# Performance work log

Hardware: AMD Instinct MI355X
Metric: run time of the kernel (lower is better)

Reference implementation:

```python
import jax, jax.numpy as jnp
from jax import lax
import numpy as np

IN_F, H1, OUT_F, P = 128, 64, 64, 0.25
B, T = 64, 2048


def setup_inputs() -> dict:
    key = jax.random.key(0)
    ks = jax.random.split(key, 12)
    def w(k, shape, fan_in):
        return jax.random.normal(k, shape, dtype=jnp.float32) / np.sqrt(fan_in).astype(np.float32)
    x = jax.random.normal(ks[0], (B, T, IN_F), dtype=jnp.float32)
    # PyTorch LSTM param layout: W_ih [4H, in], W_hh [4H, H], gate order i,f,g,o
    W_ih1 = w(ks[1], (4 * H1, IN_F), IN_F)
    W_hh1 = w(ks[2], (4 * H1, H1), H1)
    b_ih1 = jnp.zeros((4 * H1,), jnp.float32)
    b_hh1 = jnp.zeros((4 * H1,), jnp.float32)
    W_ih2 = w(ks[3], (4 * OUT_F, H1), H1)
    W_hh2 = w(ks[4], (4 * OUT_F, OUT_F), OUT_F)
    b_ih2 = jnp.zeros((4 * OUT_F,), jnp.float32)
    b_hh2 = jnp.zeros((4 * OUT_F,), jnp.float32)
    # Variational (locked) dropout masks: one per sequence, shared across timesteps,
    # inverted-dropout pre-scaled by 1/(1-p).
    keep = 1.0 - P
    mask1 = (jax.random.bernoulli(ks[5], keep, (B, H1)).astype(jnp.float32) / keep)
    mask2 = (jax.random.bernoulli(ks[6], keep, (B, OUT_F)).astype(jnp.float32) / keep)
    return {"x": x, "W_ih1": W_ih1, "W_hh1": W_hh1, "b_ih1": b_ih1, "b_hh1": b_hh1,
            "W_ih2": W_ih2, "W_hh2": W_hh2, "b_ih2": b_ih2, "b_hh2": b_hh2,
            "mask1": mask1, "mask2": mask2}


def _lstm(x, W_ih, W_hh, b_ih, b_hh):
    # x: [B,T,I]; returns all hidden states [B,T,H]
    Bd = x.shape[0]
    H = W_hh.shape[1]
    # Precompute input contribution for all timesteps (one big GEMM).
    xg = jnp.einsum('bti,gi->btg', x, W_ih) + b_ih + b_hh  # [B,T,4H]
    W_hh_T = W_hh.T  # [H,4H]
    def step(carry, xg_t):
        h, c = carry
        g = xg_t + h @ W_hh_T
        i, f, gg, o = jnp.split(g, 4, axis=-1)
        c = jax.nn.sigmoid(f) * c + jax.nn.sigmoid(i) * jnp.tanh(gg)
        h = jax.nn.sigmoid(o) * jnp.tanh(c)
        return (h, c), h
    h0 = jnp.zeros((Bd, H), x.dtype)
    c0 = jnp.zeros((Bd, H), x.dtype)
    _, hs = lax.scan(step, (h0, c0), jnp.swapaxes(xg, 0, 1))
    return jnp.swapaxes(hs, 0, 1)


def reference(x, W_ih1, W_hh1, b_ih1, b_hh1, W_ih2, W_hh2, b_ih2, b_hh2, mask1, mask2):
    out = _lstm(x, W_ih1, W_hh1, b_ih1, b_hh1) * mask1[:, None, :]
    out = _lstm(out, W_ih2, W_hh2, b_ih2, b_hh2) * mask2[:, None, :]
    return jax.nn.relu(out)
```

## Files before the change

kernel.cpp:

```cpp
#include <hip/hip_runtime.h>
#include <hip/hip_bf16.h>

#define BB 64
#define TT 2048
#define INF 128
#define HH 64
#define GG 256

__device__ __forceinline__ float sigm(float x) { return 1.0f / (1.0f + __expf(-x)); }
__device__ __forceinline__ float tanh_f(float x) {
  float e = __expf(2.0f * x);
  return 1.0f - 2.0f / (e + 1.0f);
}
__device__ __forceinline__ float bcast(float v, int l) {
  return __uint_as_float(__builtin_amdgcn_readlane(__float_as_uint(v), l));
}


#define WL1(I)                                                                  \
  { float4 a = p[lane * 16 + (I)];                                              \
    wi[4*(I)] = a.x; wi[4*(I)+1] = a.y; wi[4*(I)+2] = a.z; wi[4*(I)+3] = a.w;   \
    float4 c = p[(64 + lane) * 16 + (I)];                                       \
    wf[4*(I)] = c.x; wf[4*(I)+1] = c.y; wf[4*(I)+2] = c.z; wf[4*(I)+3] = c.w;   \
    float4 d = p[(128 + lane) * 16 + (I)];                                      \
    wg[4*(I)] = d.x; wg[4*(I)+1] = d.y; wg[4*(I)+2] = d.z; wg[4*(I)+3] = d.w;   \
    float4 e = p[(192 + lane) * 16 + (I)];                                      \
    wo[4*(I)] = e.x; wo[4*(I)+1] = e.y; wo[4*(I)+2] = e.z; wo[4*(I)+3] = e.w; }
#define WL4(I) WL1(I) WL1((I)+1) WL1((I)+2) WL1((I)+3)
#define WLOAD WL4(0) WL4(4) WL4(8) WL4(12)

#define D1(K)                                              \
  { float hk = bcast(hv, (K));                             \
    ai = fmaf(hk, wi[(K)], ai); af = fmaf(hk, wf[(K)], af);\
    ag = fmaf(hk, wg[(K)], ag); ao = fmaf(hk, wo[(K)], ao); }
#define D8(K) D1(K) D1((K)+1) D1((K)+2) D1((K)+3) D1((K)+4) D1((K)+5) D1((K)+6) D1((K)+7)
#define DOT64 D8(0) D8(8) D8(16) D8(24) D8(32) D8(40) D8(48) D8(56)

#define YW1(I) { float4 a_ = Wp[t * 32 + (I)];                                   \
    wr[4*(I)] = a_.x; wr[4*(I)+1] = a_.y; wr[4*(I)+2] = a_.z; wr[4*(I)+3] = a_.w; }
#define YW4(I) YW1(I) YW1((I)+1) YW1((I)+2) YW1((I)+3)
#define YWLOAD YW4(0) YW4(4) YW4(8) YW4(12) YW4(16) YW4(20) YW4(24) YW4(28)

#define YD1(L)                                                   \
  { float xa = bcast(curx, (L)); float xb = bcast(cury, (L));    \
    ae = fmaf(xa, wr[2*(L)], ae); ao = fmaf(xb, wr[2*(L)+1], ao); }
#define YD8(L) YD1(L) YD1((L)+1) YD1((L)+2) YD1((L)+3) YD1((L)+4) YD1((L)+5) YD1((L)+6) YD1((L)+7)
#define YDOT64 YD8(0) YD8(8) YD8(16) YD8(24) YD8(32) YD8(40) YD8(48) YD8(56)

__global__ __launch_bounds__(256, 1) void xgemm(const float* __restrict__ X,
                                                const float* __restrict__ W,
                                                const float* __restrict__ bi,
                                                const float* __restrict__ bh,
                                                float* __restrict__ XG) {
  const int t = threadIdx.x;
  const int lane = t & 63;
  const long m0 = (long)blockIdx.x * 256;

  float wr[INF];
  const float4* Wp = (const float4*)W;
  YWLOAD
  const float bias = bi[t] + bh[t];

  const float2* Xp = (const float2*)X;
  float2 cur = Xp[(size_t)m0 * 64 + lane];
  float2 nx1 = Xp[(size_t)(m0 + 1) * 64 + lane];

  for (int mi = 0; mi < 256; ++mi) {
    const long m = m0 + mi;
    float2 nx2 = make_float2(0.f, 0.f);
    if (mi + 2 < 256) nx2 = Xp[(size_t)(m + 2) * 64 + lane];

    const float curx = cur.x, cury = cur.y;
    float ae = bias, ao = 0.f;
    YDOT64
    XG[(size_t)m * GG + t] = ae + ao;
    cur = nx1; nx1 = nx2;
  }
}

__global__ __attribute__((amdgpu_flat_work_group_size(256, 256),
                          amdgpu_waves_per_eu(1, 1)))
void lstm2(const float* __restrict__ XG,
           const float* __restrict__ Whh1,
           const float* __restrict__ Wih2,
           const float* __restrict__ Whh2,
           const float* __restrict__ bi2,
           const float* __restrict__ bh2,
           const float* __restrict__ m1g,
           const float* __restrict__ m2g,
           float* __restrict__ out) {
  const int b = blockIdx.x;
  const int wid = threadIdx.x >> 6;
  const int lane = threadIdx.x & 63;

  __shared__ int f_h1, f_xe, f_xo, f_2;
  __shared__ __align__(16) float x2buf[8][HH];
  __shared__ __align__(16) float a2xbuf[8][GG];

  if (threadIdx.x == 0) { f_h1 = 0; f_xe = 0; f_xo = 0; f_2 = 0; }
  __syncthreads();

#define WAITC(seen, flag, tgt)                                  \
  do {                                                          \
    if ((seen) < (tgt)) {                                       \
      while (((seen) = *(volatile int*)&(flag)) < (tgt)) {}     \
    }                                                           \
    asm volatile("" ::: "memory");                              \
  } while (0)
#define PUBLISH(flag, val)                                      \
  do {                                                          \
    asm volatile("s_waitcnt lgkmcnt(0)" ::: "memory");          \
    if (lane == 0) *(volatile int*)&(flag) = (val);             \
  } while (0)

  if (wid == 0) {
    float wi[HH], wf[HH], wg[HH], wo[HH];
    const float4* p = (const float4*)Whh1;
    WLOAD
    const float m1 = m1g[b * HH + lane];
    const float* xgp = XG + (size_t)b * TT * GG;

    float cur0 = xgp[lane], cur1 = xgp[64 + lane], cur2 = xgp[128 + lane], cur3 = xgp[192 + lane];
    float n10 = xgp[GG + lane], n11 = xgp[GG + 64 + lane], n12 = xgp[GG + 128 + lane], n13 = xgp[GG + 192 + lane];

    float h1 = 0.f, c1 = 0.f;
    int sxe = 0, sxo = 0;
    for (int s = 0; s < TT; ++s) {
      float n20 = 0.f, n21 = 0.f, n22 = 0.f, n23 = 0.f;
      if (s + 2 < TT) {
        const float* q = xgp + (size_t)(s + 2) * GG;
        n20 = q[lane]; n21 = q[64 + lane]; n22 = q[128 + lane]; n23 = q[192 + lane];
      }

      const float hv = h1;
      float ai = cur0, af = cur1, ag = cur2, ao = cur3;
      DOT64
      c1 = sigm(af) * c1 + sigm(ai) * tanh_f(ag);
      h1 = sigm(ao) * tanh_f(c1);

      if (s & 1) { WAITC(sxo, f_xo, s - 7); }
      else       { WAITC(sxe, f_xe, s - 7); }
      x2buf[s & 7][lane] = h1 * m1;
      PUBLISH(f_h1, s + 1);

      cur0 = n10; cur1 = n11; cur2 = n12; cur3 = n13;
      n10 = n20; n11 = n21; n12 = n22; n13 = n23;
    }
  } else if (wid == 3) {
    float wi[HH], wf[HH], wg[HH], wo[HH];
    const float4* p = (const float4*)Whh2;
    WLOAD
    const float m2v = m2g[b * HH + lane];
    float* ob = out + (size_t)b * TT * HH;

    float h2 = 0.f, c2 = 0.f;
    int sxe = 0, sxo = 0;
    for (int s = 0; s < TT; ++s) {
      if (s & 1) { WAITC(sxo, f_xo, s + 1); }
      else       { WAITC(sxe, f_xe, s + 1); }
      const float pi = a2xbuf[s & 7][lane];
      const float pf = a2xbuf[s & 7][64 + lane];
      const float pg = a2xbuf[s & 7][128 + lane];
      const float po = a2xbuf[s & 7][192 + lane];

      const float hv = h2;
      float ai = 0.f, af = 0.f, ag = 0.f, ao = 0.f;
      DOT64
      ai += pi; af += pf; ag += pg; ao += po;

      c2 = sigm(af) * c2 + sigm(ai) * tanh_f(ag);
      h2 = sigm(ao) * tanh_f(c2);
      PUBLISH(f_2, s + 1);
      ob[(size_t)s * HH + lane] = fmaxf(h2 * m2v, 0.f);
    }
  } else {
    float wi[HH], wf[HH], wg[HH], wo[HH];
    const float4* p = (const float4*)Wih2;
    WLOAD
    const float bi_i = bi2[lane] + bh2[lane];
    const float bi_f = bi2[64 + lane] + bh2[64 + lane];
    const float bi_g = bi2[128 + lane] + bh2[128 + lane];
    const float bi_o = bi2[192 + lane] + bh2[192 + lane];

    const int par = wid - 1;
    volatile int* const myflag = par ? (volatile int*)&f_xo : (volatile int*)&f_xe;
    int s0 = 0, s2 = 0;
    for (int s = par; s < TT; s += 2) {
      WAITC(s0, f_h1, s + 1);
      const float hv = x2buf[s & 7][lane];

      float ai = bi_i, af = bi_f, ag = bi_g, ao = bi_o;
      DOT64

      WAITC(s2, f_2, s - 7);
      a2xbuf[s & 7][lane] = ai;
      a2xbuf[s & 7][64 + lane] = af;
      a2xbuf[s & 7][128 + lane] = ag;
      a2xbuf[s & 7][192 + lane] = ao;
      PUBLISH(*myflag, s + 1);
    }
  }
#undef WAITC
#undef PUBLISH
}

extern "C" void kernel_launch(void* const* d_in, const int* in_sizes, int n_in,
                              void* d_out, int out_size, void* d_ws, size_t ws_size,
                              hipStream_t stream) {
  (void)in_sizes; (void)n_in; (void)out_size; (void)ws_size;
  const float* x     = (const float*)d_in[0];
  const float* W_ih1 = (const float*)d_in[1];
  const float* W_hh1 = (const float*)d_in[2];
  const float* b_ih1 = (const float*)d_in[3];
  const float* b_hh1 = (const float*)d_in[4];
  const float* W_ih2 = (const float*)d_in[5];
  const float* W_hh2 = (const float*)d_in[6];
  const float* b_ih2 = (const float*)d_in[7];
  const float* b_hh2 = (const float*)d_in[8];
  const float* mask1 = (const float*)d_in[9];
  const float* mask2 = (const float*)d_in[10];
  float* out = (float*)d_out;

  float* xg1 = (float*)d_ws;

  xgemm<<<dim3(BB * TT / 256), dim3(256), 0, stream>>>(x, W_ih1, b_ih1, b_hh1, xg1);
  lstm2<<<dim3(BB), dim3(256), 0, stream>>>(xg1, W_hh1, W_ih2, W_hh2, b_ih2, b_hh2,
                                            mask1, mask2, out);
}
```

Before: 2.442 ms.

## Pack two batch sequences per block to co-schedule waves on each SIMD

```diff
diff --git a/kernel.cpp b/kernel.cpp
--- a/kernel.cpp
+++ b/kernel.cpp
@@ -78,8 +78,7 @@
   }
 }
 
-__global__ __attribute__((amdgpu_flat_work_group_size(256, 256),
-                          amdgpu_waves_per_eu(1, 1)))
+__global__ __launch_bounds__(512, 1)
 void lstm2(const float* __restrict__ XG,
            const float* __restrict__ Whh1,
            const float* __restrict__ Wih2,
@@ -89,15 +88,22 @@
            const float* __restrict__ m1g,
            const float* __restrict__ m2g,
            float* __restrict__ out) {
-  const int b = blockIdx.x;
+  const int bA = 2 * blockIdx.x;
+  const int bB = 2 * blockIdx.x + 1;
   const int wid = threadIdx.x >> 6;
   const int lane = threadIdx.x & 63;
 
-  __shared__ int f_h1, f_xe, f_xo, f_2;
-  __shared__ __align__(16) float x2buf[8][HH];
-  __shared__ __align__(16) float a2xbuf[8][GG];
-
-  if (threadIdx.x == 0) { f_h1 = 0; f_xe = 0; f_xo = 0; f_2 = 0; }
+  __shared__ int f_h1A, f_xeA, f_xoA, f_2A;
+  __shared__ int f_h1B, f_xeB, f_xoB, f_2B;
+  __shared__ __align__(16) float x2bufA[8][HH];
+  __shared__ __align__(16) float a2xbufA[8][GG];
+  __shared__ __align__(16) float x2bufB[8][HH];
+  __shared__ __align__(16) float a2xbufB[8][GG];
+
+  if (threadIdx.x == 0) {
+    f_h1A = 0; f_xeA = 0; f_xoA = 0; f_2A = 0;
+    f_h1B = 0; f_xeB = 0; f_xoB = 0; f_2B = 0;
+  }
   __syncthreads();
 
 #define WAITC(seen, flag, tgt)                                  \
@@ -117,8 +123,8 @@
     float wi[HH], wf[HH], wg[HH], wo[HH];
     const float4* p = (const float4*)Whh1;
     WLOAD
-    const float m1 = m1g[b * HH + lane];
-    const float* xgp = XG + (size_t)b * TT * GG;
+    const float m1 = m1g[bA * HH + lane];
+    const float* xgp = XG + (size_t)bA * TT * GG;
 
     float cur0 = xgp[lane], cur1 = xgp[64 + lane], cur2 = xgp[128 + lane], cur3 = xgp[192 + lane];
     float n10 = xgp[GG + lane], n11 = xgp[GG + 64 + lane], n12 = xgp[GG + 128 + lane], n13 = xgp[GG + 192 + lane];
@@ -138,10 +144,10 @@
       c1 = sigm(af) * c1 + sigm(ai) * tanh_f(ag);
       h1 = sigm(ao) * tanh_f(c1);
 
-      if (s & 1) { WAITC(sxo, f_xo, s - 7); }
-      else       { WAITC(sxe, f_xe, s - 7); }
-      x2buf[s & 7][lane] = h1 * m1;
-      PUBLISH(f_h1, s + 1);
+      if (s & 1) { WAITC(sxo, f_xoA, s - 7); }
+      else       { WAITC(sxe, f_xeA, s - 7); }
+      x2bufA[s & 7][lane] = h1 * m1;
+      PUBLISH(f_h1A, s + 1);
 
       cur0 = n10; cur1 = n11; cur2 = n12; cur3 = n13;
       n10 = n20; n11 = n21; n12 = n22; n13 = n23;
@@ -150,18 +156,18 @@
     float wi[HH], wf[HH], wg[HH], wo[HH];
     const float4* p = (const float4*)Whh2;
     WLOAD
-    const float m2v = m2g[b * HH + lane];
-    float* ob = out + (size_t)b * TT * HH;
+    const float m2v = m2g[bA * HH + lane];
+    float* ob = out + (size_t)bA * TT * HH;
 
     float h2 = 0.f, c2 = 0.f;
     int sxe = 0, sxo = 0;
     for (int s = 0; s < TT; ++s) {
-      if (s & 1) { WAITC(sxo, f_xo, s + 1); }
-      else       { WAITC(sxe, f_xe, s + 1); }
-      const float pi = a2xbuf[s & 7][lane];
-      const float pf = a2xbuf[s & 7][64 + lane];
-      const float pg = a2xbuf[s & 7][128 + lane];
-      const float po = a2xbuf[s & 7][192 + lane];
+      if (s & 1) { WAITC(sxo, f_xoA, s + 1); }
+      else       { WAITC(sxe, f_xeA, s + 1); }
+      const float pi = a2xbufA[s & 7][lane];
+      const float pf = a2xbufA[s & 7][64 + lane];
+      const float pg = a2xbufA[s & 7][128 + lane];
+      const float po = a2xbufA[s & 7][192 + lane];
 
       const float hv = h2;
       float ai = 0.f, af = 0.f, ag = 0.f, ao = 0.f;
@@ -170,10 +176,10 @@
 
       c2 = sigm(af) * c2 + sigm(ai) * tanh_f(ag);
       h2 = sigm(ao) * tanh_f(c2);
-      PUBLISH(f_2, s + 1);
+      PUBLISH(f_2A, s + 1);
       ob[(size_t)s * HH + lane] = fmaxf(h2 * m2v, 0.f);
     }
-  } else {
+  } else if (wid == 1) {
     float wi[HH], wf[HH], wg[HH], wo[HH];
     const float4* p = (const float4*)Wih2;
     WLOAD
@@ -182,22 +188,144 @@
     const float bi_g = bi2[128 + lane] + bh2[128 + lane];
     const float bi_o = bi2[192 + lane] + bh2[192 + lane];
 
-    const int par = wid - 1;
-    volatile int* const myflag = par ? (volatile int*)&f_xo : (volatile int*)&f_xe;
     int s0 = 0, s2 = 0;
-    for (int s = par; s < TT; s += 2) {
-      WAITC(s0, f_h1, s + 1);
-      const float hv = x2buf[s & 7][lane];
-
+    for (int s = 0; s < TT; s += 2) {
+      WAITC(s0, f_h1A, s + 1);
+      const float hv = x2bufA[s & 7][lane];
       float ai = bi_i, af = bi_f, ag = bi_g, ao = bi_o;
       DOT64
-
-      WAITC(s2, f_2, s - 7);
-      a2xbuf[s & 7][lane] = ai;
-      a2xbuf[s & 7][64 + lane] = af;
-      a2xbuf[s & 7][128 + lane] = ag;
-      a2xbuf[s & 7][192 + lane] = ao;
-      PUBLISH(*myflag, s + 1);
+      WAITC(s2, f_2A, s - 7);
+      a2xbufA[s & 7][lane] = ai;
+      a2xbufA[s & 7][64 + lane] = af;
+      a2xbufA[s & 7][128 + lane] = ag;
+      a2xbufA[s & 7][192 + lane] = ao;
+      PUBLISH(f_xeA, s + 1);
+    }
+  } else if (wid == 2) {
+    float wi[HH], wf[HH], wg[HH], wo[HH];
+    const float4* p = (const float4*)Wih2;
+    WLOAD
+    const float bi_i = bi2[lane] + bh2[lane];
+    const float bi_f = bi2[64 + lane] + bh2[64 + lane];
+    const float bi_g = bi2[128 + lane] + bh2[128 + lane];
+    const float bi_o = bi2[192 + lane] + bh2[192 + lane];
+
+    int s0 = 0, s2 = 0;
+    for (int s = 1; s < TT; s += 2) {
+      WAITC(s0, f_h1A, s + 1);
+      const float hv = x2bufA[s & 7][lane];
+      float ai = bi_i, af = bi_f, ag = bi_g, ao = bi_o;
+      DOT64
+      WAITC(s2, f_2A, s - 7);
+      a2xbufA[s & 7][lane] = ai;
+      a2xbufA[s & 7][64 + lane] = af;
+      a2xbufA[s & 7][128 + lane] = ag;
+      a2xbufA[s & 7][192 + lane] = ao;
+      PUBLISH(f_xoA, s + 1);
+    }
+  } else if (wid == 4) {
+    float wi[HH], wf[HH], wg[HH], wo[HH];
+    const float4* p = (const float4*)Whh1;
+    WLOAD
+    const float m1 = m1g[bB * HH + lane];
+    const float* xgp = XG + (size_t)bB * TT * GG;
+
+    float cur0 = xgp[lane], cur1 = xgp[64 + lane], cur2 = xgp[128 + lane], cur3 = xgp[192 + lane];
+    float n10 = xgp[GG + lane], n11 = xgp[GG + 64 + lane], n12 = xgp[GG + 128 + lane], n13 = xgp[GG + 192 + lane];
+
+    float h1 = 0.f, c1 = 0.f;
+    int sxe = 0, sxo = 0;
+    for (int s = 0; s < TT; ++s) {
+      float n20 = 0.f, n21 = 0.f, n22 = 0.f, n23 = 0.f;
+      if (s + 2 < TT) {
+        const float* q = xgp + (size_t)(s + 2) * GG;
+        n20 = q[lane]; n21 = q[64 + lane]; n22 = q[128 + lane]; n23 = q[192 + lane];
+      }
+
+      const float hv = h1;
+      float ai = cur0, af = cur1, ag = cur2, ao = cur3;
+      DOT64
+      c1 = sigm(af) * c1 + sigm(ai) * tanh_f(ag);
+      h1 = sigm(ao) * tanh_f(c1);
+
+      if (s & 1) { WAITC(sxo, f_xoB, s - 7); }
+      else       { WAITC(sxe, f_xeB, s - 7); }
+      x2bufB[s & 7][lane] = h1 * m1;
+      PUBLISH(f_h1B, s + 1);
+
+      cur0 = n10; cur1 = n11; cur2 = n12; cur3 = n13;
+      n10 = n20; n11 = n21; n12 = n22; n13 = n23;
+    }
+  } else if (wid == 7) {
+    float wi[HH], wf[HH], wg[HH], wo[HH];
+    const float4* p = (const float4*)Whh2;
+    WLOAD
+    const float m2v = m2g[bB * HH + lane];
+    float* ob = out + (size_t)bB * TT * HH;
+
+    float h2 = 0.f, c2 = 0.f;
+    int sxe = 0, sxo = 0;
+    for (int s = 0; s < TT; ++s) {
+      if (s & 1) { WAITC(sxo, f_xoB, s + 1); }
+      else       { WAITC(sxe, f_xeB, s + 1); }
+      const float pi = a2xbufB[s & 7][lane];
+      const float pf = a2xbufB[s & 7][64 + lane];
+      const float pg = a2xbufB[s & 7][128 + lane];
+      const float po = a2xbufB[s & 7][192 + lane];
+
+      const float hv = h2;
+      float ai = 0.f, af = 0.f, ag = 0.f, ao = 0.f;
+      DOT64
+      ai += pi; af += pf; ag += pg; ao += po;
+
+      c2 = sigm(af) * c2 + sigm(ai) * tanh_f(ag);
+      h2 = sigm(ao) * tanh_f(c2);
+      PUBLISH(f_2B, s + 1);
+      ob[(size_t)s * HH + lane] = fmaxf(h2 * m2v, 0.f);
+    }
+  } else if (wid == 5) {
+    float wi[HH], wf[HH], wg[HH], wo[HH];
+    const float4* p = (const float4*)Wih2;
+    WLOAD
+    const float bi_i = bi2[lane] + bh2[lane];
+    const float bi_f = bi2[64 + lane] + bh2[64 + lane];
+    const float bi_g = bi2[128 + lane] + bh2[128 + lane];
+    const float bi_o = bi2[192 + lane] + bh2[192 + lane];
+
+    int s0 = 0, s2 = 0;
+    for (int s = 0; s < TT; s += 2) {
+      WAITC(s0, f_h1B, s + 1);
+      const float hv = x2bufB[s & 7][lane];
+      float ai = bi_i, af = bi_f, ag = bi_g, ao = bi_o;
+      DOT64
+      WAITC(s2, f_2B, s - 7);
+      a2xbufB[s & 7][lane] = ai;
+      a2xbufB[s & 7][64 + lane] = af;
+      a2xbufB[s & 7][128 + lane] = ag;
+      a2xbufB[s & 7][192 + lane] = ao;
+      PUBLISH(f_xeB, s + 1);
+    }
+  } else {
+    float wi[HH], wf[HH], wg[HH], wo[HH];
+    const float4* p = (const float4*)Wih2;
+    WLOAD
+    const float bi_i = bi2[lane] + bh2[lane];
+    const float bi_f = bi2[64 + lane] + bh2[64 + lane];
+    const float bi_g = bi2[128 + lane] + bh2[128 + lane];
+    const float bi_o = bi2[192 + lane] + bh2[192 + lane];
+
+    int s0 = 0, s2 = 0;
+    for (int s = 1; s < TT; s += 2) {
+      WAITC(s0, f_h1B, s + 1);
+      const float hv = x2bufB[s & 7][lane];
+      float ai = bi_i, af = bi_f, ag = bi_g, ao = bi_o;
+      DOT64
+      WAITC(s2, f_2B, s - 7);
+      a2xbufB[s & 7][lane] = ai;
+      a2xbufB[s & 7][64 + lane] = af;
+      a2xbufB[s & 7][128 + lane] = ag;
+      a2xbufB[s & 7][192 + lane] = ao;
+      PUBLISH(f_xoB, s + 1);
     }
   }
 #undef WAITC
@@ -224,6 +352,6 @@
   float* xg1 = (float*)d_ws;
 
   xgemm<<<dim3(BB * TT / 256), dim3(256), 0, stream>>>(x, W_ih1, b_ih1, b_hh1, xg1);
-  lstm2<<<dim3(BB), dim3(256), 0, stream>>>(xg1, W_hh1, W_ih2, W_hh2, b_ih2, b_hh2,
-                                            mask1, mask2, out);
-}
+  lstm2<<<dim3(BB / 2), dim3(512), 0, stream>>>(xg1, W_hh1, W_ih2, W_hh2,
+                                                b_ih2, b_hh2, mask1, mask2, out);
+}
```

New measurement: 4.779 ms. +95.7%, slower.

## Use packed FP32 FMAs and LDS-broadcast hidden state in LSTM recurrences

Applied to the files above, without the earlier changes.

```diff
diff --git a/kernel.cpp b/kernel.cpp
--- a/kernel.cpp
+++ b/kernel.cpp
@@ -7,6 +7,14 @@
 #define HH 64
 #define GG 256
 
+typedef float v2f __attribute__((ext_vector_type(2)));
+__device__ __forceinline__ v2f mk2(float x, float y) { v2f r; r.x = x; r.y = y; return r; }
+#if __has_builtin(__builtin_elementwise_fma)
+#define VFMA(a, b, c) __builtin_elementwise_fma((a), (b), (c))
+#else
+#define VFMA(a, b, c) ((a) * (b) + (c))
+#endif
+
 __device__ __forceinline__ float sigm(float x) { return 1.0f / (1.0f + __expf(-x)); }
 __device__ __forceinline__ float tanh_f(float x) {
   float e = __expf(2.0f * x);
@@ -17,33 +25,37 @@
 }
 
 
-#define WL1(I)                                                                  \
-  { float4 a = p[lane * 16 + (I)];                                              \
-    wi[4*(I)] = a.x; wi[4*(I)+1] = a.y; wi[4*(I)+2] = a.z; wi[4*(I)+3] = a.w;   \
-    float4 c = p[(64 + lane) * 16 + (I)];                                       \
-    wf[4*(I)] = c.x; wf[4*(I)+1] = c.y; wf[4*(I)+2] = c.z; wf[4*(I)+3] = c.w;   \
-    float4 d = p[(128 + lane) * 16 + (I)];                                      \
-    wg[4*(I)] = d.x; wg[4*(I)+1] = d.y; wg[4*(I)+2] = d.z; wg[4*(I)+3] = d.w;   \
-    float4 e = p[(192 + lane) * 16 + (I)];                                      \
-    wo[4*(I)] = e.x; wo[4*(I)+1] = e.y; wo[4*(I)+2] = e.z; wo[4*(I)+3] = e.w; }
-#define WL4(I) WL1(I) WL1((I)+1) WL1((I)+2) WL1((I)+3)
-#define WLOAD WL4(0) WL4(4) WL4(8) WL4(12)
-
-#define D1(K)                                              \
-  { float hk = bcast(hv, (K));                             \
-    ai = fmaf(hk, wi[(K)], ai); af = fmaf(hk, wf[(K)], af);\
-    ag = fmaf(hk, wg[(K)], ag); ao = fmaf(hk, wo[(K)], ao); }
-#define D8(K) D1(K) D1((K)+1) D1((K)+2) D1((K)+3) D1((K)+4) D1((K)+5) D1((K)+6) D1((K)+7)
-#define DOT64 D8(0) D8(8) D8(16) D8(24) D8(32) D8(40) D8(48) D8(56)
+#define PWL(I)                                                                  \
+  { float4 a_ = p[lane * 16 + (I)];                                     \
+    float4 c_ = p[(64 + lane) * 16 + (I)];                              \
+    float4 d_ = p[(128 + lane) * 16 + (I)];                             \
+    float4 e_ = p[(192 + lane) * 16 + (I)];                             \
+    wIF[4*(I)]   = mk2(a_.x, c_.x); wGO[4*(I)]   = mk2(d_.x, e_.x);             \
+    wIF[4*(I)+1] = mk2(a_.y, c_.y); wGO[4*(I)+1] = mk2(d_.y, e_.y);             \
+    wIF[4*(I)+2] = mk2(a_.z, c_.z); wGO[4*(I)+2] = mk2(d_.z, e_.z);             \
+    wIF[4*(I)+3] = mk2(a_.w, c_.w); wGO[4*(I)+3] = mk2(d_.w, e_.w); }
+#define PWL4(I) PWL(I) PWL((I)+1) PWL((I)+2) PWL((I)+3)
+#define PWLOAD PWL4(0) PWL4(4) PWL4(8) PWL4(12)
+
+#define PKQ(J)                                                        \
+  { const float4 hq = hb[(J)];                                        \
+    const v2f h0 = mk2(hq.x, hq.x), h1 = mk2(hq.y, hq.y);             \
+    const v2f h2 = mk2(hq.z, hq.z), h3 = mk2(hq.w, hq.w);             \
+    aIF = VFMA(h0, wIF[4*(J)],   aIF); aGO = VFMA(h0, wGO[4*(J)],   aGO); \
+    aIF = VFMA(h1, wIF[4*(J)+1], aIF); aGO = VFMA(h1, wGO[4*(J)+1], aGO); \
+    aIF = VFMA(h2, wIF[4*(J)+2], aIF); aGO = VFMA(h2, wGO[4*(J)+2], aGO); \
+    aIF = VFMA(h3, wIF[4*(J)+3], aIF); aGO = VFMA(h3, wGO[4*(J)+3], aGO); }
+#define PKDOT PKQ(0) PKQ(1) PKQ(2) PKQ(3) PKQ(4) PKQ(5) PKQ(6) PKQ(7)   \
+              PKQ(8) PKQ(9) PKQ(10) PKQ(11) PKQ(12) PKQ(13) PKQ(14) PKQ(15)
 
 #define YW1(I) { float4 a_ = Wp[t * 32 + (I)];                                   \
-    wr[4*(I)] = a_.x; wr[4*(I)+1] = a_.y; wr[4*(I)+2] = a_.z; wr[4*(I)+3] = a_.w; }
+    wp[2*(I)] = mk2(a_.x, a_.y); wp[2*(I)+1] = mk2(a_.z, a_.w); }
 #define YW4(I) YW1(I) YW1((I)+1) YW1((I)+2) YW1((I)+3)
 #define YWLOAD YW4(0) YW4(4) YW4(8) YW4(12) YW4(16) YW4(20) YW4(24) YW4(28)
 
 #define YD1(L)                                                   \
   { float xa = bcast(curx, (L)); float xb = bcast(cury, (L));    \
-    ae = fmaf(xa, wr[2*(L)], ae); ao = fmaf(xb, wr[2*(L)+1], ao); }
+    acc2 = VFMA(mk2(xa, xb), wp[(L)], acc2); }
 #define YD8(L) YD1(L) YD1((L)+1) YD1((L)+2) YD1((L)+3) YD1((L)+4) YD1((L)+5) YD1((L)+6) YD1((L)+7)
 #define YDOT64 YD8(0) YD8(8) YD8(16) YD8(24) YD8(32) YD8(40) YD8(48) YD8(56)
 
@@ -56,7 +68,7 @@
   const int lane = t & 63;
   const long m0 = (long)blockIdx.x * 256;
 
-  float wr[INF];
+  v2f wp[64];
   const float4* Wp = (const float4*)W;
   YWLOAD
   const float bias = bi[t] + bh[t];
@@ -71,15 +83,14 @@
     if (mi + 2 < 256) nx2 = Xp[(size_t)(m + 2) * 64 + lane];
 
     const float curx = cur.x, cury = cur.y;
-    float ae = bias, ao = 0.f;
+    v2f acc2 = mk2(bias, 0.f);
     YDOT64
-    XG[(size_t)m * GG + t] = ae + ao;
+    XG[(size_t)m * GG + t] = acc2.x + acc2.y;
     cur = nx1; nx1 = nx2;
   }
 }
 
-__global__ __attribute__((amdgpu_flat_work_group_size(256, 256),
-                          amdgpu_waves_per_eu(1, 1)))
+__global__ __launch_bounds__(256, 1)
 void lstm2(const float* __restrict__ XG,
            const float* __restrict__ Whh1,
            const float* __restrict__ Wih2,
@@ -96,6 +107,8 @@
   __shared__ int f_h1, f_xe, f_xo, f_2;
   __shared__ __align__(16) float x2buf[8][HH];
   __shared__ __align__(16) float a2xbuf[8][GG];
+  __shared__ __align__(16) float hrep1[2][HH];
+  __shared__ __align__(16) float hrep2[2][HH];
 
   if (threadIdx.x == 0) { f_h1 = 0; f_xe = 0; f_xo = 0; f_2 = 0; }
   __syncthreads();
@@ -114,11 +127,13 @@
   } while (0)
 
   if (wid == 0) {
-    float wi[HH], wf[HH], wg[HH], wo[HH];
+    v2f wIF[HH], wGO[HH];
     const float4* p = (const float4*)Whh1;
-    WLOAD
+    PWLOAD
     const float m1 = m1g[b * HH + lane];
     const float* xgp = XG + (size_t)b * TT * GG;
+
+    hrep1[0][lane] = 0.f;
 
     float cur0 = xgp[lane], cur1 = xgp[64 + lane], cur2 = xgp[128 + lane], cur3 = xgp[192 + lane];
     float n10 = xgp[GG + lane], n11 = xgp[GG + 64 + lane], n12 = xgp[GG + 128 + lane], n13 = xgp[GG + 192 + lane];
@@ -132,26 +147,29 @@
         n20 = q[lane]; n21 = q[64 + lane]; n22 = q[128 + lane]; n23 = q[192 + lane];
       }
 
-      const float hv = h1;
-      float ai = cur0, af = cur1, ag = cur2, ao = cur3;
-      DOT64
-      c1 = sigm(af) * c1 + sigm(ai) * tanh_f(ag);
-      h1 = sigm(ao) * tanh_f(c1);
+      const float4* hb = (const float4*)(&hrep1[s & 1][0]);
+      v2f aIF = mk2(cur0, cur1), aGO = mk2(cur2, cur3);
+      PKDOT
+      c1 = sigm(aIF.y) * c1 + sigm(aIF.x) * tanh_f(aGO.x);
+      h1 = sigm(aGO.y) * tanh_f(c1);
 
       if (s & 1) { WAITC(sxo, f_xo, s - 7); }
       else       { WAITC(sxe, f_xe, s - 7); }
       x2buf[s & 7][lane] = h1 * m1;
+      hrep1[(s + 1) & 1][lane] = h1;
       PUBLISH(f_h1, s + 1);
 
       cur0 = n10; cur1 = n11; cur2 = n12; cur3 = n13;
       n10 = n20; n11 = n21; n12 = n22; n13 = n23;
     }
   } else if (wid == 3) {
-    float wi[HH], wf[HH], wg[HH], wo[HH];
+    v2f wIF[HH], wGO[HH];
     const float4* p = (const float4*)Whh2;
-    WLOAD
+    PWLOAD
     const float m2v = m2g[b * HH + lane];
     float* ob = out + (size_t)b * TT * HH;
+
+    hrep2[0][lane] = 0.f;
 
     float h2 = 0.f, c2 = 0.f;
     int sxe = 0, sxo = 0;
@@ -163,41 +181,42 @@
       const float pg = a2xbuf[s & 7][128 + lane];
       const float po = a2xbuf[s & 7][192 + lane];
 
-      const float hv = h2;
-      float ai = 0.f, af = 0.f, ag = 0.f, ao = 0.f;
-      DOT64
-      ai += pi; af += pf; ag += pg; ao += po;
-
-      c2 = sigm(af) * c2 + sigm(ai) * tanh_f(ag);
-      h2 = sigm(ao) * tanh_f(c2);
+      const float4* hb = (const float4*)(&hrep2[s & 1][0]);
+      v2f aIF = mk2(0.f, 0.f), aGO = mk2(0.f, 0.f);
+      PKDOT
+      aIF = aIF + mk2(pi, pf);
+      aGO = aGO + mk2(pg, po);
+
+      c2 = sigm(aIF.y) * c2 + sigm(aIF.x) * tanh_f(aGO.x);
+      h2 = sigm(aGO.y) * tanh_f(c2);
+      hrep2[(s + 1) & 1][lane] = h2;
       PUBLISH(f_2, s + 1);
       ob[(size_t)s * HH + lane] = fmaxf(h2 * m2v, 0.f);
     }
   } else {
-    float wi[HH], wf[HH], wg[HH], wo[HH];
+    v2f wIF[HH], wGO[HH];
     const float4* p = (const float4*)Wih2;
-    WLOAD
+    PWLOAD
     const float bi_i = bi2[lane] + bh2[lane];
     const float bi_f = bi2[64 + lane] + bh2[64 + lane];
     const float bi_g = bi2[128 + lane] + bh2[128 + lane];
     const float bi_o = bi2[192 + lane] + bh2[192 + lane];
 
     const int par = wid - 1;
-    volatile int* const myflag = par ? (volatile int*)&f_xo : (volatile int*)&f_xe;
     int s0 = 0, s2 = 0;
     for (int s = par; s < TT; s += 2) {
       WAITC(s0, f_h1, s + 1);
-      const float hv = x2buf[s & 7][lane];
-
-      float ai = bi_i, af = bi_f, ag = bi_g, ao = bi_o;
-      DOT64
+      const float4* hb = (const float4*)(&x2buf[s & 7][0]);
+      v2f aIF = mk2(bi_i, bi_f), aGO = mk2(bi_g, bi_o);
+      PKDOT
 
       WAITC(s2, f_2, s - 7);
-      a2xbuf[s & 7][lane] = ai;
-      a2xbuf[s & 7][64 + lane] = af;
-      a2xbuf[s & 7][128 + lane] = ag;
-      a2xbuf[s & 7][192 + lane] = ao;
-      PUBLISH(*myflag, s + 1);
+      a2xbuf[s & 7][lane] = aIF.x;
+      a2xbuf[s & 7][64 + lane] = aIF.y;
+      a2xbuf[s & 7][128 + lane] = aGO.x;
+      a2xbuf[s & 7][192 + lane] = aGO.y;
+      if (par) { PUBLISH(f_xo, s + 1); }
+      else     { PUBLISH(f_xe, s + 1); }
     }
   }
 #undef WAITC
@@ -224,6 +243,6 @@
   float* xg1 = (float*)d_ws;
 
   xgemm<<<dim3(BB * TT / 256), dim3(256), 0, stream>>>(x, W_ih1, b_ih1, b_hh1, xg1);
-  lstm2<<<dim3(BB), dim3(256), 0, stream>>>(xg1, W_hh1, W_ih2, W_hh2, b_ih2, b_hh2,
-                                            mask1, mask2, out);
-}
+  lstm2<<<dim3(BB), dim3(256), 0, stream>>>(xg1, W_hh1, W_ih2, W_hh2,
+                                            b_ih2, b_hh2, mask1, mask2, out);
+}
```

Result: slower. 2.657 ms (+8.8%).
